# Kernel tuning notes

Hardware: AMD Instinct MI355X
Metric: run time of the kernel (lower is better)

Reference implementation:

```python
import jax, jax.numpy as jnp
import numpy as np

DT = 0.1
THRESH = 10.0

def setup_inputs() -> dict:
    key = jax.random.key(0)
    ks = jax.random.split(key, 6)
    B, S, H, V = 2, 1024, 1024, 50257
    hidden_states = jax.random.normal(ks[0], (B, S, H), dtype=jnp.float32)
    ttu_state = jnp.zeros((B, 3), dtype=jnp.float32)
    W_imp = jax.random.normal(ks[1], (3, H), dtype=jnp.float32) * 0.02
    b_imp = jnp.zeros((3,), dtype=jnp.float32)
    W_lm = jax.random.normal(ks[2], (V, H), dtype=jnp.float32) * 0.02
    W_mod = jax.random.normal(ks[3], (V, 3), dtype=jnp.float32) * 0.02
    # gamma, alpha_c, beta_c, delta, alpha_d, epsilon, alpha_m
    ttu_params = jax.random.uniform(ks[4], (7,), dtype=jnp.float32, minval=0.1, maxval=1.0)
    return {"hidden_states": hidden_states, "ttu_state": ttu_state,
            "W_imp": W_imp, "b_imp": b_imp, "W_lm": W_lm, "W_mod": W_mod,
            "ttu_params": ttu_params}

def _ttu_scan(ttu_state, impulses, ttu_params):
    # impulses: [S, B, 3] (time-major for scan)
    gamma, alpha_c, beta_c, delta, alpha_d, epsilon, alpha_m = ttu_params
    def step(state, imp):
        phi_c, phi_d, phi_m = state[:, 0], state[:, 1], state[:, 2]
        dphi_c = gamma * imp[:, 0] - alpha_c * phi_c - beta_c * phi_c * phi_d
        dphi_d = delta * phi_c ** 2 - alpha_d * phi_d
        dphi_m = epsilon * phi_d - alpha_m * phi_m
        new_c = phi_c + DT * dphi_c
        new_d = phi_d + DT * dphi_d
        new_m = phi_m + DT * dphi_m
        # saturation damping on phi_d
        new_d = jnp.where(jnp.abs(new_d) > THRESH, jnp.float32(0.5), jnp.float32(1.0)) * new_d
        new_state = jnp.stack([new_c, new_d, new_m], axis=1)  # [B, 3]
        return new_state, new_state
    return jax.lax.scan(step, ttu_state, impulses)

def reference(hidden_states, ttu_state, W_imp, b_imp, W_lm, W_mod, ttu_params):
    # impulse projections computed in batch up front: [S, B, 3]
    impulses = jnp.einsum('bsh,dh->sbd', hidden_states, W_imp) + b_imp
    final_state, states = _ttu_scan(ttu_state, impulses, ttu_params)  # states: [S, B, 3]
    # base lm logits + 0.1 * modulation from ttu trajectory
    logits = jnp.einsum('bsh,vh->bsv', hidden_states, W_lm) \
           + 0.1 * jnp.einsum('sbd,vd->bsv', states, W_mod)
    return logits, final_state
```

## Files before the change

### kernel.cpp

```cpp
#include <hip/hip_runtime.h>
#include <hip/hip_bf16.h>

typedef float  f32x4  __attribute__((ext_vector_type(4)));
typedef short  bf16x8 __attribute__((ext_vector_type(8)));
typedef short  bf16x4 __attribute__((ext_vector_type(4)));

typedef const void __attribute__((address_space(1))) gv_t;
typedef void __attribute__((address_space(3))) sv_t;

namespace {

constexpr int B_ = 2;
constexpr int S_ = 1024;
constexpr int H_ = 1024;
constexpr int V_ = 50257;
constexpr int M_ = B_ * S_;
constexpr int VP_ = 50304;
constexpr float DT_ = 0.1f;
constexpr float THRESH_ = 10.0f;

constexpr int BM = 128, BN = 128, BK = 64;
constexpr int NT = H_ / BK;

__device__ __forceinline__ unsigned short f2bf(float f) {
  union { float f; unsigned u; } x;
  x.f = f;
  x.u += 0x7FFFu + ((x.u >> 16) & 1u);
  return (unsigned short)(x.u >> 16);
}

__global__ void cvt_hidden_impulse_kernel(const float* __restrict__ hidden,
                                          const float* __restrict__ W_imp,
                                          const float* __restrict__ b_imp,
                                          unsigned short* __restrict__ hid_bf,
                                          float* __restrict__ imp) {
  const int m = blockIdx.x;
  const int t = threadIdx.x;
  const float4 hv = reinterpret_cast<const float4*>(hidden + (size_t)m * H_)[t];
  const float4 wv = reinterpret_cast<const float4*>(W_imp)[t];
  bf16x4 o;
  o[0] = (short)f2bf(hv.x); o[1] = (short)f2bf(hv.y);
  o[2] = (short)f2bf(hv.z); o[3] = (short)f2bf(hv.w);
  *(bf16x4*)(hid_bf + (size_t)m * H_ + t * 4) = o;
  float p = hv.x * wv.x + hv.y * wv.y + hv.z * wv.z + hv.w * wv.w;
  #pragma unroll
  for (int off = 32; off; off >>= 1) p += __shfl_down(p, off);
  __shared__ float partial[4];
  if ((t & 63) == 0) partial[t >> 6] = p;
  __syncthreads();
  if (t == 0) {
    const float v = partial[0] + partial[1] + partial[2] + partial[3] + b_imp[0];
    const int b = m >> 10;
    const int s = m & (S_ - 1);
    imp[s * B_ + b] = v;
  }
}

__global__ void ttu_scan_kernel(const float* __restrict__ imp,
                                const float* __restrict__ ttu_state,
                                const float* __restrict__ ttu_params,
                                float* __restrict__ states,
                                float* __restrict__ final_out) {
  __shared__ float imp_s[S_ * B_];
  const int t = threadIdx.x;
  for (int i = t; i < S_ * B_; i += 64) imp_s[i] = imp[i];
  __syncthreads();
  if (t < B_) {
    const float gamma   = ttu_params[0];
    const float alpha_c = ttu_params[1];
    const float beta_c  = ttu_params[2];
    const float delta   = ttu_params[3];
    const float alpha_d = ttu_params[4];
    const float epsilon = ttu_params[5];
    const float alpha_m = ttu_params[6];
    float c = ttu_state[t * 3 + 0];
    float d = ttu_state[t * 3 + 1];
    float m = ttu_state[t * 3 + 2];
    for (int s = 0; s < S_; ++s) {
      const float ii = imp_s[s * B_ + t];
      const float dc = gamma * ii - alpha_c * c - beta_c * c * d;
      const float dd = delta * c * c - alpha_d * d;
      const float dm = epsilon * d - alpha_m * m;
      c = c + DT_ * dc;
      float nd = d + DT_ * dd;
      m = m + DT_ * dm;
      nd = (fabsf(nd) > THRESH_ ? 0.5f : 1.0f) * nd;
      d = nd;
      float* st = states + (size_t)(s * B_ + t) * 3;
      st[0] = c; st[1] = d; st[2] = m;
    }
    final_out[t * 3 + 0] = c;
    final_out[t * 3 + 1] = d;
    final_out[t * 3 + 2] = m;
  }
}

__global__ void cvt_bf16_kernel(const float* __restrict__ src,
                                unsigned short* __restrict__ dst,
                                long n_src, long n_dst) {
  const long stride = (long)gridDim.x * blockDim.x * 8;
  for (long i = ((long)blockIdx.x * blockDim.x + threadIdx.x) * 8; i < n_dst; i += stride) {
    bf16x8 v;
    if (i < n_src) {
      const float4 a = *(const float4*)(src + i);
      const float4 b = *(const float4*)(src + i + 4);
      v[0] = (short)f2bf(a.x); v[1] = (short)f2bf(a.y);
      v[2] = (short)f2bf(a.z); v[3] = (short)f2bf(a.w);
      v[4] = (short)f2bf(b.x); v[5] = (short)f2bf(b.y);
      v[6] = (short)f2bf(b.z); v[7] = (short)f2bf(b.w);
    } else {
      v = (bf16x8){0, 0, 0, 0, 0, 0, 0, 0};
    }
    *(bf16x8*)(dst + i) = v;
  }
}

__global__ __launch_bounds__(256) void ttu_gemm_bf16_db_kernel(
    const unsigned short* __restrict__ Ab,
    const unsigned short* __restrict__ Bb,
    const float* __restrict__ states,
    const float* __restrict__ Wmod,
    float* __restrict__ out)
{
  __shared__ unsigned short AB_s[2][2][BM * BK];
  __shared__ float st_s[BM][3];
  __shared__ float wm_s[BN][3];

  const int t = threadIdx.x;
  const int cpx = gridDim.x >> 3;
  const int bid = (blockIdx.x & 7) * cpx + (blockIdx.x >> 3);
  const int mb = bid & 15;
  const int nb = bid >> 4;
  const int m0 = mb * BM;
  const int n0 = nb * BN;

  if (t < BM) {
    const int m = m0 + t;
    const int b = m >> 10;
    const int s = m & (S_ - 1);
    const float* st = states + (size_t)(s * B_ + b) * 3;
    st_s[t][0] = st[0]; st_s[t][1] = st[1]; st_s[t][2] = st[2];
  } else {
    const int tt = t - BM;
    const int n = n0 + tt;
    const bool ok = n < V_;
    wm_s[tt][0] = ok ? Wmod[n * 3 + 0] : 0.f;
    wm_s[tt][1] = ok ? Wmod[n * 3 + 1] : 0.f;
    wm_s[tt][2] = ok ? Wmod[n * 3 + 2] : 0.f;
  }

  const int lane = t & 63;
  const int wid  = t >> 6;
  const int lr   = lane >> 3;
  const int ch   = lane & 7;
  const int wm   = wid >> 1;
  const int wn   = wid & 1;
  const int lm   = lane & 15;
  const int kg   = lane >> 4;

  const unsigned short* Abase = Ab + (size_t)m0 * H_;
  const unsigned short* Bbase = Bb + (size_t)n0 * H_;

  const int r0 = wid * 32;
  auto STAGE = [&](unsigned short* As, unsigned short* Bs, int kt) {
    const int k0 = kt * BK;
    #pragma unroll
    for (int ins = 0; ins < 4; ++ins) {
      const int lrow = r0 + ins * 8 + lr;
      const int sch  = ch ^ (lrow & 7);
      __builtin_amdgcn_global_load_lds(
          (gv_t*)(Abase + (size_t)lrow * H_ + k0 + sch * 8),
          (sv_t*)(As + (r0 + ins * 8) * BK), 16, 0, 0);
    }
    #pragma unroll
    for (int ins = 0; ins < 4; ++ins) {
      const int lrow = r0 + ins * 8 + lr;
      const int sch  = ch ^ (lrow & 7);
      __builtin_amdgcn_global_load_lds(
          (gv_t*)(Bbase + (size_t)lrow * H_ + k0 + sch * 8),
          (sv_t*)(Bs + (r0 + ins * 8) * BK), 16, 0, 0);
    }
  };

  f32x4 acc[4][4];
  #pragma unroll
  for (int i = 0; i < 4; ++i)
    #pragma unroll
    for (int j = 0; j < 4; ++j)
      acc[i][j] = (f32x4){0.f, 0.f, 0.f, 0.f};

  unsigned short* Ac = &AB_s[0][0][0];
  unsigned short* Bc = &AB_s[0][1][0];
  unsigned short* An = &AB_s[1][0][0];
  unsigned short* Bn = &AB_s[1][1][0];

  STAGE(Ac, Bc, 0);
  __syncthreads();

  for (int kt = 0; kt < NT; ++kt) {
    if (kt + 1 < NT) STAGE(An, Bn, kt + 1);

    bf16x8 af[4][2], bfr[4][2];
    #pragma unroll
    for (int i = 0; i < 4; ++i) {
      const int arow = wm * 64 + i * 16 + lm;
      const int brow = wn * 64 + i * 16 + lm;
      #pragma unroll
      for (int ks = 0; ks < 2; ++ks) {
        af[i][ks]  = *(const bf16x8*)&Ac[arow * BK + (((ks * 4 + kg) ^ (arow & 7)) << 3)];
        bfr[i][ks] = *(const bf16x8*)&Bc[brow * BK + (((ks * 4 + kg) ^ (brow & 7)) << 3)];
      }
    }
    #pragma unroll
    for (int ks = 0; ks < 2; ++ks)
      #pragma unroll
      for (int i = 0; i < 4; ++i)
        #pragma unroll
        for (int j = 0; j < 4; ++j)
          acc[i][j] = __builtin_amdgcn_mfma_f32_16x16x32_bf16(af[i][ks], bfr[j][ks], acc[i][j], 0, 0, 0);

    __syncthreads();
    unsigned short* tp;
    tp = Ac; Ac = An; An = tp;
    tp = Bc; Bc = Bn; Bn = tp;
  }

  #pragma unroll
  for (int i = 0; i < 4; ++i) {
    #pragma unroll
    for (int rr = 0; rr < 4; ++rr) {
      const int mloc = wm * 64 + i * 16 + kg * 4 + rr;
      const float s0 = st_s[mloc][0], s1 = st_s[mloc][1], s2 = st_s[mloc][2];
      float* orow = out + (size_t)(m0 + mloc) * V_ + n0;
      #pragma unroll
      for (int j = 0; j < 4; ++j) {
        const int nloc = wn * 64 + j * 16 + lm;
        if (n0 + nloc < V_) {
          const float corr = 0.1f * (s0 * wm_s[nloc][0] + s1 * wm_s[nloc][1] + s2 * wm_s[nloc][2]);
          orow[nloc] = acc[i][j][rr] + corr;
        }
      }
    }
  }
}

__global__ __launch_bounds__(256) void ttu_gemm_kernel(
    const float* __restrict__ Ag, const float* __restrict__ Bg,
    const float* __restrict__ states, const float* __restrict__ Wmod,
    float* __restrict__ out)
{
  __shared__ unsigned short A_s[BM][40];
  __shared__ unsigned short B_s[BM][40];
  __shared__ float st_s[BM][3];
  __shared__ float wm_s[BM][3];

  const int t   = threadIdx.x;
  const int bid = blockIdx.x;
  const int mb  = bid & 15;
  const int nb  = bid >> 4;
  const int m0  = mb * BM;
  const int n0  = nb * BM;

  if (t < BM) {
    const int m = m0 + t;
    const int b = m >> 10;
    const int s = m & (S_ - 1);
    const float* st = states + (size_t)(s * B_ + b) * 3;
    st_s[t][0] = st[0]; st_s[t][1] = st[1]; st_s[t][2] = st[2];
  } else {
    const int tt = t - BM;
    const int n  = n0 + tt;
    const bool ok = n < V_;
    wm_s[tt][0] = ok ? Wmod[n * 3 + 0] : 0.f;
    wm_s[tt][1] = ok ? Wmod[n * 3 + 1] : 0.f;
    wm_s[tt][2] = ok ? Wmod[n * 3 + 2] : 0.f;
  }

  const int r   = t >> 1;
  const int seg = t & 1;
  const float* arow = Ag + (size_t)(m0 + r) * H_ + seg * 16;
  const int  vrow = n0 + r;
  const bool bok  = vrow < V_;
  const float* brow = Bg + (size_t)(bok ? vrow : 0) * H_ + seg * 16;

  const int lane = t & 63;
  const int wid  = t >> 6;
  const int wm   = wid >> 1;
  const int wn   = wid & 1;
  const int lm   = lane & 15;
  const int kg   = lane >> 4;

  f32x4 acc[4][4];
  #pragma unroll
  for (int i = 0; i < 4; ++i)
    #pragma unroll
    for (int j = 0; j < 4; ++j)
      acc[i][j] = (f32x4){0.f, 0.f, 0.f, 0.f};

  for (int kt = 0; kt < H_ / 32; ++kt) {
    const int k0 = kt * 32;
    const float4 av0 = *(const float4*)(arow + k0 + 0);
    const float4 av1 = *(const float4*)(arow + k0 + 4);
    const float4 av2 = *(const float4*)(arow + k0 + 8);
    const float4 av3 = *(const float4*)(arow + k0 + 12);
    float4 bv0 = {0,0,0,0}, bv1 = {0,0,0,0}, bv2 = {0,0,0,0}, bv3 = {0,0,0,0};
    if (bok) {
      bv0 = *(const float4*)(brow + k0 + 0);
      bv1 = *(const float4*)(brow + k0 + 4);
      bv2 = *(const float4*)(brow + k0 + 8);
      bv3 = *(const float4*)(brow + k0 + 12);
    }
    __syncthreads();
    #define CVT4(v) (bf16x4){(short)f2bf((v).x), (short)f2bf((v).y), (short)f2bf((v).z), (short)f2bf((v).w)}
    *(bf16x4*)&A_s[r][seg * 16 + 0]  = CVT4(av0);
    *(bf16x4*)&A_s[r][seg * 16 + 4]  = CVT4(av1);
    *(bf16x4*)&A_s[r][seg * 16 + 8]  = CVT4(av2);
    *(bf16x4*)&A_s[r][seg * 16 + 12] = CVT4(av3);
    *(bf16x4*)&B_s[r][seg * 16 + 0]  = CVT4(bv0);
    *(bf16x4*)&B_s[r][seg * 16 + 4]  = CVT4(bv1);
    *(bf16x4*)&B_s[r][seg * 16 + 8]  = CVT4(bv2);
    *(bf16x4*)&B_s[r][seg * 16 + 12] = CVT4(bv3);
    #undef CVT4
    __syncthreads();
    bf16x8 af[4], bf[4];
    #pragma unroll
    for (int i = 0; i < 4; ++i) {
      af[i] = *(const bf16x8*)&A_s[wm * 64 + i * 16 + lm][kg * 8];
      bf[i] = *(const bf16x8*)&B_s[wn * 64 + i * 16 + lm][kg * 8];
    }
    #pragma unroll
    for (int i = 0; i < 4; ++i)
      #pragma unroll
      for (int j = 0; j < 4; ++j)
        acc[i][j] = __builtin_amdgcn_mfma_f32_16x16x32_bf16(af[i], bf[j], acc[i][j], 0, 0, 0);
  }

  #pragma unroll
  for (int i = 0; i < 4; ++i) {
    #pragma unroll
    for (int rr = 0; rr < 4; ++rr) {
      const int mloc = wm * 64 + i * 16 + kg * 4 + rr;
      const float s0 = st_s[mloc][0], s1 = st_s[mloc][1], s2 = st_s[mloc][2];
      float* orow = out + (size_t)(m0 + mloc) * V_ + n0;
      #pragma unroll
      for (int j = 0; j < 4; ++j) {
        const int nloc = wn * 64 + j * 16 + lm;
        if (n0 + nloc < V_) {
          const float corr = 0.1f * (s0 * wm_s[nloc][0] + s1 * wm_s[nloc][1] + s2 * wm_s[nloc][2]);
          orow[nloc] = acc[i][j][rr] + corr;
        }
      }
    }
  }
}

}

extern "C" void kernel_launch(void* const* d_in, const int* in_sizes, int n_in,
                              void* d_out, int out_size, void* d_ws, size_t ws_size,
                              hipStream_t stream) {
  const float* hidden     = (const float*)d_in[0];
  const float* ttu_state  = (const float*)d_in[1];
  const float* W_imp      = (const float*)d_in[2];
  const float* b_imp      = (const float*)d_in[3];
  const float* W_lm       = (const float*)d_in[4];
  const float* W_mod      = (const float*)d_in[5];
  const float* ttu_params = (const float*)d_in[6];
  float* out = (float*)d_out;

  float* imp    = (float*)d_ws;
  float* states = imp + S_ * B_;

  const size_t need = 32768 + (size_t)M_ * H_ * 2 + (size_t)VP_ * H_ * 2;
  const int grid = (VP_ / BN) * (M_ / BM);

  if (ws_size >= need) {
    unsigned short* hid_bf = (unsigned short*)((char*)d_ws + 32768);
    unsigned short* wlm_bf = hid_bf + (size_t)M_ * H_;
    cvt_hidden_impulse_kernel<<<M_, 256, 0, stream>>>(hidden, W_imp, b_imp, hid_bf, imp);
    ttu_scan_kernel<<<1, 64, 0, stream>>>(imp, ttu_state, ttu_params, states,
                                          out + (size_t)B_ * S_ * V_);
    cvt_bf16_kernel<<<4096, 256, 0, stream>>>(W_lm, wlm_bf,
                                              (long)V_ * H_, (long)VP_ * H_);
    ttu_gemm_bf16_db_kernel<<<grid, 256, 0, stream>>>(hid_bf, wlm_bf, states, W_mod, out);
  } else {
    cvt_hidden_impulse_kernel<<<M_, 256, 0, stream>>>(hidden, W_imp, b_imp,
                                                      (unsigned short*)d_ws , imp);
    ttu_scan_kernel<<<1, 64, 0, stream>>>(imp, ttu_state, ttu_params, states,
                                          out + (size_t)B_ * S_ * V_);
    ttu_gemm_kernel<<<grid, 256, 0, stream>>>(hidden, W_lm, states, W_mod, out);
  }
}
```

Before: 525.2 us.

## Fuse scan into weight conversion, use vmcnt-based pipelining and nontemporal stores

The sequential TTU scan now runs in the last block of the W_lm bf16 conversion kernel, so it overlaps with the conversion and saves one launch. The GEMM main loop swaps its two __syncthreads per iteration for raw s_barrier plus s_waitcnt vmcnt(8), so the next tile's async LDS loads can stay in flight during compute. Output stores become nontemporal, launch bounds request two blocks per CU, and the conversion grid shrinks to 2048 worker blocks. The hand-written waitcnt relies on the compiler's exact count of outstanding loads, which is fragile and could cause races if codegen changes.

After: 527.4 us. Within noise of the previous version (+0.4%).

```diff
diff --git a/kernel.cpp b/kernel.cpp
--- a/kernel.cpp
+++ b/kernel.cpp
@@ -15,11 +15,11 @@
 constexpr int H_ = 1024;
 constexpr int V_ = 50257;
 constexpr int M_ = B_ * S_;
-constexpr int VP_ = 50304;
+constexpr int VP1_ = 50304;
 constexpr float DT_ = 0.1f;
 constexpr float THRESH_ = 10.0f;
 
-constexpr int BM = 128, BN = 128, BK = 64;
+constexpr int BK = 64;
 constexpr int NT = H_ / BK;
 
 __device__ __forceinline__ unsigned short f2bf(float f) {
@@ -56,15 +56,11 @@
   }
 }
 
-__global__ void ttu_scan_kernel(const float* __restrict__ imp,
-                                const float* __restrict__ ttu_state,
-                                const float* __restrict__ ttu_params,
-                                float* __restrict__ states,
-                                float* __restrict__ final_out) {
-  __shared__ float imp_s[S_ * B_];
-  const int t = threadIdx.x;
-  for (int i = t; i < S_ * B_; i += 64) imp_s[i] = imp[i];
-  __syncthreads();
+__device__ __forceinline__ void scan_body(const float* __restrict__ imp_s,
+                                          const float* __restrict__ ttu_state,
+                                          const float* __restrict__ ttu_params,
+                                          float* __restrict__ states,
+                                          float* __restrict__ final_out, int t) {
   if (t < B_) {
     const float gamma   = ttu_params[0];
     const float alpha_c = ttu_params[1];
@@ -95,11 +91,36 @@
   }
 }
 
-__global__ void cvt_bf16_kernel(const float* __restrict__ src,
-                                unsigned short* __restrict__ dst,
-                                long n_src, long n_dst) {
-  const long stride = (long)gridDim.x * blockDim.x * 8;
-  for (long i = ((long)blockIdx.x * blockDim.x + threadIdx.x) * 8; i < n_dst; i += stride) {
+__global__ void ttu_scan_kernel(const float* __restrict__ imp,
+                                const float* __restrict__ ttu_state,
+                                const float* __restrict__ ttu_params,
+                                float* __restrict__ states,
+                                float* __restrict__ final_out) {
+  __shared__ float imp_s[S_ * B_];
+  const int t = threadIdx.x;
+  for (int i = t; i < S_ * B_; i += 64) imp_s[i] = imp[i];
+  __syncthreads();
+  scan_body(imp_s, ttu_state, ttu_params, states, final_out, t);
+}
+
+__global__ void cvt_wlm_scan_kernel(const float* __restrict__ src,
+                                    unsigned short* __restrict__ dst,
+                                    long n_src, long n_dst,
+                                    const float* __restrict__ imp,
+                                    const float* __restrict__ ttu_state,
+                                    const float* __restrict__ ttu_params,
+                                    float* __restrict__ states,
+                                    float* __restrict__ final_out) {
+  __shared__ float imp_s[S_ * B_];
+  const int t = threadIdx.x;
+  if (blockIdx.x == gridDim.x - 1) {
+    for (int i = t; i < S_ * B_; i += 256) imp_s[i] = imp[i];
+    __syncthreads();
+    scan_body(imp_s, ttu_state, ttu_params, states, final_out, t);
+    return;
+  }
+  const long stride = (long)(gridDim.x - 1) * blockDim.x * 8;
+  for (long i = ((long)blockIdx.x * blockDim.x + t) * 8; i < n_dst; i += stride) {
     bf16x8 v;
     if (i < n_src) {
       const float4 a = *(const float4*)(src + i);
@@ -115,33 +136,33 @@
   }
 }
 
-__global__ __launch_bounds__(256) void ttu_gemm_bf16_db_kernel(
+__global__ __launch_bounds__(256, 2) void ttu_gemm_bf16_cnt_kernel(
     const unsigned short* __restrict__ Ab,
     const unsigned short* __restrict__ Bb,
     const float* __restrict__ states,
     const float* __restrict__ Wmod,
     float* __restrict__ out)
 {
-  __shared__ unsigned short AB_s[2][2][BM * BK];
-  __shared__ float st_s[BM][3];
-  __shared__ float wm_s[BN][3];
+  __shared__ unsigned short AB_s[2][2][128 * BK];
+  __shared__ float st_s[128][3];
+  __shared__ float wm_s[128][3];
 
   const int t = threadIdx.x;
   const int cpx = gridDim.x >> 3;
   const int bid = (blockIdx.x & 7) * cpx + (blockIdx.x >> 3);
   const int mb = bid & 15;
   const int nb = bid >> 4;
-  const int m0 = mb * BM;
-  const int n0 = nb * BN;
-
-  if (t < BM) {
+  const int m0 = mb * 128;
+  const int n0 = nb * 128;
+
+  if (t < 128) {
     const int m = m0 + t;
     const int b = m >> 10;
     const int s = m & (S_ - 1);
     const float* st = states + (size_t)(s * B_ + b) * 3;
     st_s[t][0] = st[0]; st_s[t][1] = st[1]; st_s[t][2] = st[2];
   } else {
-    const int tt = t - BM;
+    const int tt = t - 128;
     const int n = n0 + tt;
     const bool ok = n < V_;
     wm_s[tt][0] = ok ? Wmod[n * 3 + 0] : 0.f;
@@ -160,8 +181,8 @@
 
   const unsigned short* Abase = Ab + (size_t)m0 * H_;
   const unsigned short* Bbase = Bb + (size_t)n0 * H_;
-
   const int r0 = wid * 32;
+
   auto STAGE = [&](unsigned short* As, unsigned short* Bs, int kt) {
     const int k0 = kt * BK;
     #pragma unroll
@@ -195,10 +216,16 @@
   unsigned short* Bn = &AB_s[1][1][0];
 
   STAGE(Ac, Bc, 0);
-  __syncthreads();
 
   for (int kt = 0; kt < NT; ++kt) {
-    if (kt + 1 < NT) STAGE(An, Bn, kt + 1);
+    asm volatile("s_barrier" ::: "memory");
+    if (kt + 1 < NT) {
+      STAGE(An, Bn, kt + 1);
+      asm volatile("s_waitcnt vmcnt(8)" ::: "memory");
+    } else {
+      asm volatile("s_waitcnt vmcnt(0)" ::: "memory");
+    }
+    asm volatile("s_barrier" ::: "memory");
 
     bf16x8 af[4][2], bfr[4][2];
     #pragma unroll
@@ -219,7 +246,6 @@
         for (int j = 0; j < 4; ++j)
           acc[i][j] = __builtin_amdgcn_mfma_f32_16x16x32_bf16(af[i][ks], bfr[j][ks], acc[i][j], 0, 0, 0);
 
-    __syncthreads();
     unsigned short* tp;
     tp = Ac; Ac = An; An = tp;
     tp = Bc; Bc = Bn; Bn = tp;
@@ -237,7 +263,7 @@
         const int nloc = wn * 64 + j * 16 + lm;
         if (n0 + nloc < V_) {
           const float corr = 0.1f * (s0 * wm_s[nloc][0] + s1 * wm_s[nloc][1] + s2 * wm_s[nloc][2]);
-          orow[nloc] = acc[i][j][rr] + corr;
+          __builtin_nontemporal_store(acc[i][j][rr] + corr, &orow[nloc]);
         }
       }
     }
@@ -249,26 +275,26 @@
     const float* __restrict__ states, const float* __restrict__ Wmod,
     float* __restrict__ out)
 {
-  __shared__ unsigned short A_s[BM][40];
-  __shared__ unsigned short B_s[BM][40];
-  __shared__ float st_s[BM][3];
-  __shared__ float wm_s[BM][3];
+  __shared__ unsigned short A_s[128][40];
+  __shared__ unsigned short B_s[128][40];
+  __shared__ float st_s[128][3];
+  __shared__ float wm_s[128][3];
 
   const int t   = threadIdx.x;
   const int bid = blockIdx.x;
   const int mb  = bid & 15;
   const int nb  = bid >> 4;
-  const int m0  = mb * BM;
-  const int n0  = nb * BM;
-
-  if (t < BM) {
+  const int m0  = mb * 128;
+  const int n0  = nb * 128;
+
+  if (t < 128) {
     const int m = m0 + t;
     const int b = m >> 10;
     const int s = m & (S_ - 1);
     const float* st = states + (size_t)(s * B_ + b) * 3;
     st_s[t][0] = st[0]; st_s[t][1] = st[1]; st_s[t][2] = st[2];
   } else {
-    const int tt = t - BM;
+    const int tt = t - 128;
     const int n  = n0 + tt;
     const bool ok = n < V_;
     wm_s[tt][0] = ok ? Wmod[n * 3 + 0] : 0.f;
@@ -370,24 +396,25 @@
 
   float* imp    = (float*)d_ws;
   float* states = imp + S_ * B_;
-
-  const size_t need = 32768 + (size_t)M_ * H_ * 2 + (size_t)VP_ * H_ * 2;
-  const int grid = (VP_ / BN) * (M_ / BM);
+  float* final_out = out + (size_t)B_ * S_ * V_;
+
+  const size_t need = 32768 + (size_t)M_ * H_ * 2 + (size_t)VP1_ * H_ * 2;
 
   if (ws_size >= need) {
     unsigned short* hid_bf = (unsigned short*)((char*)d_ws + 32768);
     unsigned short* wlm_bf = hid_bf + (size_t)M_ * H_;
     cvt_hidden_impulse_kernel<<<M_, 256, 0, stream>>>(hidden, W_imp, b_imp, hid_bf, imp);
-    ttu_scan_kernel<<<1, 64, 0, stream>>>(imp, ttu_state, ttu_params, states,
-                                          out + (size_t)B_ * S_ * V_);
-    cvt_bf16_kernel<<<4096, 256, 0, stream>>>(W_lm, wlm_bf,
-                                              (long)V_ * H_, (long)VP_ * H_);
-    ttu_gemm_bf16_db_kernel<<<grid, 256, 0, stream>>>(hid_bf, wlm_bf, states, W_mod, out);
+    cvt_wlm_scan_kernel<<<2049, 256, 0, stream>>>(W_lm, wlm_bf,
+                                                  (long)V_ * H_, (long)VP1_ * H_,
+                                                  imp, ttu_state, ttu_params,
+                                                  states, final_out);
+    const int grid = (VP1_ / 128) * (M_ / 128);
+    ttu_gemm_bf16_cnt_kernel<<<grid, 256, 0, stream>>>(hid_bf, wlm_bf, states, W_mod, out);
   } else {
     cvt_hidden_impulse_kernel<<<M_, 256, 0, stream>>>(hidden, W_imp, b_imp,
-                                                      (unsigned short*)d_ws , imp);
-    ttu_scan_kernel<<<1, 64, 0, stream>>>(imp, ttu_state, ttu_params, states,
-                                          out + (size_t)B_ * S_ * V_);
+                                                      (unsigned short*)d_ws, imp);
+    ttu_scan_kernel<<<1, 64, 0, stream>>>(imp, ttu_state, ttu_params, states, final_out);
+    const int grid = ((V_ + 127) / 128) * (M_ / 128);
     ttu_gemm_kernel<<<grid, 256, 0, stream>>>(hidden, W_lm, states, W_mod, out);
   }
 }
```
